# Kernel optimization log

Hardware: AMD Instinct MI355X
Metric: run time of the kernel (lower is better)

The kernel has to match this reference:

```python
import jax, jax.numpy as jnp
import numpy as np
from jax.scipy.special import gammaln

# Problem sizes (static)
N = 50000          # nodes
P = 200000         # paths (source->target pairs in the transitive closure)
L = 6              # edges (nodes) per path -> flat edge list length E = P*L
E = P * L
MAX_DELAY = 128
DT = 1.0
T = int(MAX_DELAY * int(1 / DT))   # expanded time window (== 128)
EPS = 1e-12


def gamma_irf(params):
    """IRF_FN entry: per-node gamma (Nash-cascade) impulse response, [N, T]."""
    a = jax.nn.softplus(params[:, 0]) + 1.0      # shape  > 1
    b = jax.nn.softplus(params[:, 1]) + 0.5      # scale  > 0.5
    t = (jnp.arange(T, dtype=jnp.float32) + 0.5) * jnp.float32(DT)  # [T]
    log_irf = ((a[:, None] - 1.0) * jnp.log(t)[None, :]
               - t[None, :] / b[:, None]
               - gammaln(a)[:, None]
               - a[:, None] * jnp.log(b)[:, None])
    return jnp.exp(log_irf) * jnp.float32(DT)    # [N, T]


def setup_inputs() -> dict:
    key = jax.random.key(0)
    k1, k2 = jax.random.split(key)
    params = jax.random.normal(k1, (N, 2), dtype=jnp.float32)
    edges_flat = jax.random.randint(k2, (E,), 0, N, dtype=jnp.int32)
    path_cumsum = jnp.arange(P + 1, dtype=jnp.int32) * L  # segment offsets into edges_flat
    return {"params": params, "edges_flat": edges_flat, "path_cumsum": path_cumsum}


def reference(params, edges_flat, path_cumsum):
    # --- irf_fn + rfft ---------------------------------------------------
    irfs = gamma_irf(params)                          # [N, T]
    irfs_freq = jnp.fft.rfft(irfs, n=T, axis=-1)      # [N, F] complex64

    # --- log_transitive_closure: product of per-edge spectra along paths -
    log_f = jnp.log(irfs_freq + EPS)                  # complex log, [N, F]
    seg_ids = jnp.searchsorted(path_cumsum[1:], jnp.arange(E, dtype=path_cumsum.dtype),
                               side="right")          # [E] path id per flat edge
    path_log = jax.ops.segment_sum(log_f[edges_flat], seg_ids, num_segments=P)  # [P, F]
    path_freq = jnp.exp(path_log)                     # product along path, [P, F]

    # coords: (source node, target node) of each path; include_index_diag appends (i, i)
    src = edges_flat[path_cumsum[:-1]]
    dst = edges_flat[path_cumsum[1:] - 1]
    diag = jnp.arange(N, dtype=edges_flat.dtype)
    coords = jnp.stack([jnp.concatenate([src, diag]),
                        jnp.concatenate([dst, diag])])              # [2, P+N]
    freq_all = jnp.concatenate([path_freq, irfs_freq], axis=0)      # [P+N, F]

    # --- irfft + postprocessing ------------------------------------------
    irfs_agg = jnp.fft.irfft(freq_all, n=T, axis=-1)  # [P+N, T]
    irfs_agg = jax.nn.relu(irfs_agg)
    # sampler.phi_k: avg-pool by factor int(1/dt) == 1 -> identity when dt=1
    irfs_agg = jnp.flip(irfs_agg, axis=-1)
    irfs_agg = irfs_agg / (jnp.sum(irfs_agg, axis=-1, keepdims=True) + EPS)
    # SparseKernel(coords, values, kernel_size=(N, N, T)) -> return its contents
    return (coords, irfs_agg)
```

## Files before the change

kernel.cpp:

```cpp
#include <hip/hip_runtime.h>
#include <hip/hip_bf16.h>

#define N_NODES 50000
#define P_PATHS 200000
#define N_ROWS  250000
#define L_EDGES 6
#define T_LEN   128
#define F_BINS  65
#define EPSF    1e-12f
#define PIF     3.14159265358979323846f
#define COORD_ELEMS ((size_t)2 * (P_PATHS + N_NODES))
#define FREQ_BYTES  ((size_t)N_NODES * F_BINS * 8)
#define ATILE_OFF   ((size_t)32 * 1024 * 1024)
#define KDIM  128
#define KPADN 128
#define ROWS_BLK 64
#define TILES ((N_ROWS + ROWS_BLK - 1) / ROWS_BLK)
#define GEMM_GRID 1024

typedef _Float16 v2h __attribute__((ext_vector_type(2)));
typedef _Float16 v8h __attribute__((ext_vector_type(8)));
typedef float    v4f __attribute__((ext_vector_type(4)));

__device__ __forceinline__ float softplus_(float x) {
    const float e = __expf(-fabsf(x));
    return fmaxf(x, 0.0f) + __logf(1.0f + e);
}

__device__ __forceinline__ float lgamma_pos_(float x) {
    const float ser = 1.000000000190015f
                    + 76.18009172947146f     / (x + 1.0f)
                    - 86.50532032941677f     / (x + 2.0f)
                    + 24.01409824083091f     / (x + 3.0f)
                    - 1.231739572450155f     / (x + 4.0f)
                    + 0.1208650973866179e-2f / (x + 5.0f)
                    - 0.5395239384953e-5f    / (x + 6.0f);
    const float tmp = x + 5.5f;
    return (x + 0.5f) * __logf(tmp) - tmp + __logf(2.5066282746310005f * ser / x);
}

__global__ void irfa49s_wgen(_Float16* __restrict__ Wt) {
    const int idx = blockIdx.x * 256 + threadIdx.x;
    if (idx >= 128 * KDIM) return;
    const int t  = idx / KDIM;
    const int kk = idx - t * KDIM;
    int j; float cj; bool is_sin;
    if (kk == 1) { j = 64; cj = 1.0f; is_sin = false; }
    else {
        j = kk >> 1;
        cj = (j == 0) ? 1.0f : 2.0f;
        is_sin = (kk & 1);
    }
    const int m = (j * t) & 127;
    const float th = (float)m * (PIF / 64.0f);
    const float tri = is_sin ? -__sinf(th) : __cosf(th);
    Wt[idx] = (_Float16)(cj * tri * (1.0f / 128.0f));
}

__global__ void irfa49s_freq(const float* __restrict__ params, _Float16* __restrict__ freqh) {
    __shared__ float sx[8][T_LEN];
    __shared__ float su[8][64];
    __shared__ float sv[8][64];
    const int tid  = threadIdx.x;
    const int slot = tid >> 5;
    const int tl   = tid & 31;
    const int n    = blockIdx.x * 8 + slot;
    _Float16* fh   = freqh + (size_t)n * KPADN;

    const float a  = softplus_(params[2 * n + 0]) + 1.0f;
    const float b  = softplus_(params[2 * n + 1]) + 0.5f;
    const float lg = lgamma_pos_(a);
    const float lb = __logf(b);
    const float rb = 1.0f / b;
    const float am1 = a - 1.0f;
    const float cst = -lg - a * lb;

    float S = 0.0f;
    #pragma unroll
    for (int j = 0; j < 4; ++j) {
        const float tc = (float)(tl + 32 * j) + 0.5f;
        const float x  = __expf(fmaf(am1, __logf(tc), fmaf(-tc, rb, cst)));
        sx[slot][tl + 32 * j] = x;
        S += x;
    }

    float s0  = S;
    float s64 = (tl & 1) ? -S : S;
    float c32 = ((tl & 3) == 0) ? S : (((tl & 3) == 2) ? -S : 0.0f);
    float s32 = ((tl & 3) == 1) ? S : (((tl & 3) == 3) ? -S : 0.0f);
    #pragma unroll
    for (int m = 16; m; m >>= 1) {
        s0  += __shfl_xor(s0, m);
        s64 += __shfl_xor(s64, m);
        c32 += __shfl_xor(c32, m);
        s32 += __shfl_xor(s32, m);
    }
    __syncthreads();

    {
        const int i1 = tl + 1;
        const float xa = sx[slot][i1], xb = sx[slot][T_LEN - i1];
        su[slot][i1] = xa + xb;
        sv[slot][i1] = xa - xb;
        if (tl < 31) {
            const int i2 = tl + 33;
            const float xc = sx[slot][i2], xd = sx[slot][T_LEN - i2];
            su[slot][i2] = xc + xd;
            sv[slot][i2] = xc - xd;
        }
    }
    __syncthreads();

    if (tl == 0) {
        v2h h;
        h[0] = (_Float16)s0;  h[1] = (_Float16)s64;    *(v2h*)(fh + 0)  = h;
        h[0] = (_Float16)c32; h[1] = (_Float16)(-s32); *(v2h*)(fh + 64) = h;
        return;
    }

    const float x0v  = sx[slot][0];
    const float x64v = sx[slot][64];
    const int   k    = tl;
    const float th   = (float)k * (PIF / 64.0f);
    const float c1 = __cosf(th), s1 = __sinf(th);
    const float c2 = 2.0f * c1 * c1 - 1.0f;
    const float s2 = 2.0f * s1 * c1;
    const float K  = 2.0f * c2;

    float ue1 = 0.0f, ue2 = 0.0f, ve1 = 0.0f, ve2 = 0.0f;
    float uo1 = 0.0f, uo2 = 0.0f, vo1 = 0.0f, vo2 = 0.0f;
    #pragma unroll
    for (int m = 31; m >= 1; --m) {
        const float2 uu = *(const float2*)&su[slot][2 * m];
        const float2 vv = *(const float2*)&sv[slot][2 * m];
        float v0;
        v0 = fmaf(K, ue1, uu.x - ue2); ue2 = ue1; ue1 = v0;
        v0 = fmaf(K, ve1, vv.x - ve2); ve2 = ve1; ve1 = v0;
        v0 = fmaf(K, uo1, uu.y - uo2); uo2 = uo1; uo1 = v0;
        v0 = fmaf(K, vo1, vv.y - vo2); vo2 = vo1; vo1 = v0;
    }
    {
        float v0;
        v0 = fmaf(K, uo1, su[slot][1] - uo2); uo2 = uo1; uo1 = v0;
        v0 = fmaf(K, vo1, sv[slot][1] - vo2); vo2 = vo1; vo1 = v0;
    }

    const float Ec = fmaf(ue1, c2, -ue2);
    const float Es = ve1 * s2;
    const float ReSu = fmaf(-uo2, c2, uo1);
    const float ImSu = uo2 * s2;
    const float Oc   = c1 * ReSu - s1 * ImSu;
    const float ReSv = fmaf(-vo2, c2, vo1);
    const float ImSv = vo2 * s2;
    const float Os   = s1 * ReSv + c1 * ImSv;

    const float base = x0v + ((k & 1) ? -x64v : x64v);
    v2h h;
    h[0] = (_Float16)(base + Ec + Oc);
    h[1] = (_Float16)(-(Es + Os));
    *(v2h*)(fh + 2 * k) = h;
    h[0] = (_Float16)(base + Ec - Oc);
    h[1] = (_Float16)(Es - Os);
    *(v2h*)(fh + 2 * (64 - k)) = h;
}

__global__ __launch_bounds__(256) void irfa49t_prod(const _Float16* __restrict__ freqh,
                                                    const int* __restrict__ edges,
                                                    _Float16* __restrict__ Atile) {
    const int gt  = blockIdx.x * 256 + threadIdx.x;
    const int row = gt >> 5;
    const int tl  = gt & 31;
    _Float16* op = Atile + (size_t)row * KDIM;

    if (row < P_PATHS) {
        const int eb = row * L_EDGES;
        v2h av[L_EDGES], bv[L_EDGES];
        #pragma unroll
        for (int j = 0; j < L_EDGES; ++j) {
            const _Float16* fh = freqh + (size_t)edges[eb + j] * KPADN;
            av[j] = *(const v2h*)(fh + 2 * tl);
            bv[j] = *(const v2h*)(fh + 64 + 2 * tl);
        }
        float p1r = 1.0f, p1i = 0.0f, p2r = 1.0f, p2i = 0.0f, q = 1.0f;
        #pragma unroll
        for (int j = 0; j < L_EDGES; ++j) {
            const float ax  = (float)av[j][0];
            const float ayr = (float)av[j][1];
            const float ay  = (tl == 0) ? 0.0f : ayr;
            float t1 = p1r * ax - p1i * ay;
            p1i      = p1r * ay + p1i * ax;
            p1r = t1;
            q *= ayr;
            const float bx = (float)bv[j][0], by = (float)bv[j][1];
            float t2 = p2r * bx - p2i * by;
            p2i      = p2r * by + p2i * bx;
            p2r = t2;
        }
        v2h h;
        h[0] = (_Float16)p1r;
        h[1] = (tl == 0) ? (_Float16)q : (_Float16)p1i;
        *(v2h*)(op + 2 * tl) = h;
        h[0] = (_Float16)p2r; h[1] = (_Float16)p2i;
        *(v2h*)(op + 64 + 2 * tl) = h;
    } else {
        const _Float16* fh = freqh + (size_t)(row - P_PATHS) * KPADN;
        *(v2h*)(op + 2 * tl)      = *(const v2h*)(fh + 2 * tl);
        *(v2h*)(op + 64 + 2 * tl) = *(const v2h*)(fh + 64 + 2 * tl);
    }
}

__global__ __launch_bounds__(256, 2) void irfa49u_gemm(const _Float16* __restrict__ Atile,
                                                       const _Float16* __restrict__ Wt,
                                                       float* __restrict__ out_agg) {
    const int tid  = threadIdx.x;
    const int wv   = tid >> 6;
    const int lane = tid & 63;
    const int tcol = lane & 15;
    const int kg   = lane >> 4;
    const int rgrp = kg * 4;

    v8h bf[4][8];
    #pragma unroll
    for (int kt = 0; kt < 4; ++kt) {
        #pragma unroll
        for (int nt = 0; nt < 8; ++nt) {
            bf[kt][nt] = *(const v8h*)&Wt[(nt * 16 + tcol) * KDIM + kt * 32 + kg * 8];
        }
    }

    for (int tile = blockIdx.x; tile < TILES; tile += GEMM_GRID) {
        const int rowa = tile * ROWS_BLK + wv * 16 + tcol;
        const _Float16* ap = Atile + (size_t)rowa * KDIM + kg * 8;

        v8h af[4];
        #pragma unroll
        for (int kt = 0; kt < 4; ++kt) af[kt] = *(const v8h*)(ap + kt * 32);

        v4f acc[8];
        #pragma unroll
        for (int nt = 0; nt < 8; ++nt) acc[nt] = (v4f){0.0f, 0.0f, 0.0f, 0.0f};

        #pragma unroll
        for (int kt = 0; kt < 4; ++kt) {
            #pragma unroll
            for (int nt = 0; nt < 8; ++nt) {
                acc[nt] = __builtin_amdgcn_mfma_f32_16x16x32_f16(af[kt], bf[kt][nt], acc[nt], 0, 0, 0);
            }
        }

        #pragma unroll
        for (int reg = 0; reg < 4; ++reg) {
            float vals[8];
            float vsum = 0.0f;
            #pragma unroll
            for (int nt = 0; nt < 8; ++nt) {
                const float v = fmaxf(acc[nt][reg], 0.0f);
                vals[nt] = v;
                vsum += v;
            }
            vsum += __shfl_xor(vsum, 1);
            vsum += __shfl_xor(vsum, 2);
            vsum += __shfl_xor(vsum, 4);
            vsum += __shfl_xor(vsum, 8);
            const int row = tile * ROWS_BLK + wv * 16 + rgrp + reg;
            if (row < N_ROWS) {
                const float inv = 1.0f / (vsum + EPSF);
                float* op = out_agg + (size_t)row * T_LEN;
                #pragma unroll
                for (int nt = 0; nt < 8; ++nt) {
                    const int t = nt * 16 + tcol;
                    op[127 - t] = vals[nt] * inv;
                }
            }
        }
    }
}

__global__ void IRFAggregator_39049842655549_kernel(const int* __restrict__ edges,
                                                    float* __restrict__ out) {
    const int M = P_PATHS + N_NODES;
    const int i = blockIdx.x * blockDim.x + threadIdx.x;
    if (i >= 2 * M) return;
    int v;
    if (i < P_PATHS) {
        v = edges[i * L_EDGES];
    } else if (i < M) {
        v = i - P_PATHS;
    } else {
        const int j = i - M;
        if (j < P_PATHS) v = edges[j * L_EDGES + L_EDGES - 1];
        else             v = j - P_PATHS;
    }
    out[i] = (float)v;
}

extern "C" void kernel_launch(void* const* d_in, const int* in_sizes, int n_in,
                              void* d_out, int out_size, void* d_ws, size_t ws_size,
                              hipStream_t stream) {
    const float* params = (const float*)d_in[0];
    const int*   edges  = (const int*)d_in[1];

    _Float16* freqh = (_Float16*)d_ws;
    _Float16* Wt    = (_Float16*)((char*)d_ws + FREQ_BYTES);
    _Float16* Atile = (_Float16*)((char*)d_ws + ATILE_OFF);
    float* out      = (float*)d_out;
    float* out_agg  = out + COORD_ELEMS;

    IRFAggregator_39049842655549_kernel<<<(int)((COORD_ELEMS + 255) / 256), 256, 0, stream>>>(edges, out);
    irfa49s_wgen<<<(128 * KDIM + 255) / 256, 256, 0, stream>>>(Wt);
    irfa49s_freq<<<N_NODES / 8, 256, 0, stream>>>(params, freqh);
    irfa49t_prod<<<(N_ROWS * 32) / 256, 256, 0, stream>>>(freqh, edges, Atile);
    irfa49u_gemm<<<GEMM_GRID, 256, 0, stream>>>(Atile, Wt, out_agg);
}
```

Measured before the change: 117.0 us.

## Compute per-node forward DFT as fp16 MFMA GEMM instead of Goertzel recurrence

Replaces the per-node shared-memory Goertzel-style forward DFT with a separate IRF generation kernel that writes fp16 time samples to a table, plus an MFMA GEMM against a precomputed cos/sin matrix to produce the spectra. This moves the scalar recurrence onto matrix cores. In exchange it adds a round trip through global memory for the time table, two extra launches, and fp16 rounding of the time samples before the transform.

```diff
diff --git a/kernel.cpp b/kernel.cpp
--- a/kernel.cpp
+++ b/kernel.cpp
@@ -12,11 +12,14 @@
 #define COORD_ELEMS ((size_t)2 * (P_PATHS + N_NODES))
 #define FREQ_BYTES  ((size_t)N_NODES * F_BINS * 8)
 #define ATILE_OFF   ((size_t)32 * 1024 * 1024)
+#define XTAB_OFF    ((size_t)96 * 1024 * 1024)
 #define KDIM  128
 #define KPADN 128
 #define ROWS_BLK 64
 #define TILES ((N_ROWS + ROWS_BLK - 1) / ROWS_BLK)
 #define GEMM_GRID 1024
+#define STILES ((N_NODES + ROWS_BLK - 1) / ROWS_BLK)
+#define SPEC_GRID 391
 
 typedef _Float16 v2h __attribute__((ext_vector_type(2)));
 typedef _Float16 v8h __attribute__((ext_vector_type(8)));
@@ -57,111 +60,89 @@
     Wt[idx] = (_Float16)(cj * tri * (1.0f / 128.0f));
 }
 
-__global__ void irfa49s_freq(const float* __restrict__ params, _Float16* __restrict__ freqh) {
-    __shared__ float sx[8][T_LEN];
-    __shared__ float su[8][64];
-    __shared__ float sv[8][64];
+__global__ void irfa49v_w2gen(_Float16* __restrict__ W2t) {
+    const int idx = blockIdx.x * 256 + threadIdx.x;
+    if (idx >= 128 * 128) return;
+    const int kk = idx >> 7;
+    const int t  = idx & 127;
+    int j; bool is_sin;
+    if (kk == 1) { j = 64; is_sin = false; }
+    else { j = kk >> 1; is_sin = (kk & 1); }
+    const int m = (j * t) & 127;
+    const float th = (float)m * (PIF / 64.0f);
+    W2t[idx] = (_Float16)(is_sin ? -__sinf(th) : __cosf(th));
+}
+
+__global__ __launch_bounds__(256) void irfa49v_xgen(const float* __restrict__ params,
+                                                    _Float16* __restrict__ xtab) {
     const int tid  = threadIdx.x;
-    const int slot = tid >> 5;
-    const int tl   = tid & 31;
-    const int n    = blockIdx.x * 8 + slot;
-    _Float16* fh   = freqh + (size_t)n * KPADN;
-
-    const float a  = softplus_(params[2 * n + 0]) + 1.0f;
-    const float b  = softplus_(params[2 * n + 1]) + 0.5f;
+    const int node = blockIdx.x * 2 + (tid >> 7);
+    const int t    = tid & 127;
+
+    const float a  = softplus_(params[2 * node + 0]) + 1.0f;
+    const float b  = softplus_(params[2 * node + 1]) + 0.5f;
     const float lg = lgamma_pos_(a);
     const float lb = __logf(b);
     const float rb = 1.0f / b;
-    const float am1 = a - 1.0f;
     const float cst = -lg - a * lb;
-
-    float S = 0.0f;
+    const float tc = (float)t + 0.5f;
+    const float x  = __expf(fmaf(a - 1.0f, __logf(tc), fmaf(-tc, rb, cst)));
+    xtab[(size_t)node * T_LEN + t] = (_Float16)x;
+}
+
+__global__ __launch_bounds__(256, 2) void irfa49v_spec(const _Float16* __restrict__ xtab,
+                                                       const _Float16* __restrict__ W2t,
+                                                       _Float16* __restrict__ freqh) {
+    const int tid  = threadIdx.x;
+    const int wv   = tid >> 6;
+    const int lane = tid & 63;
+    const int tcol = lane & 15;
+    const int kg   = lane >> 4;
+    const int rgrp = kg * 4;
+
+    v8h bf[4][8];
     #pragma unroll
-    for (int j = 0; j < 4; ++j) {
-        const float tc = (float)(tl + 32 * j) + 0.5f;
-        const float x  = __expf(fmaf(am1, __logf(tc), fmaf(-tc, rb, cst)));
-        sx[slot][tl + 32 * j] = x;
-        S += x;
-    }
-
-    float s0  = S;
-    float s64 = (tl & 1) ? -S : S;
-    float c32 = ((tl & 3) == 0) ? S : (((tl & 3) == 2) ? -S : 0.0f);
-    float s32 = ((tl & 3) == 1) ? S : (((tl & 3) == 3) ? -S : 0.0f);
-    #pragma unroll
-    for (int m = 16; m; m >>= 1) {
-        s0  += __shfl_xor(s0, m);
-        s64 += __shfl_xor(s64, m);
-        c32 += __shfl_xor(c32, m);
-        s32 += __shfl_xor(s32, m);
-    }
-    __syncthreads();
-
-    {
-        const int i1 = tl + 1;
-        const float xa = sx[slot][i1], xb = sx[slot][T_LEN - i1];
-        su[slot][i1] = xa + xb;
-        sv[slot][i1] = xa - xb;
-        if (tl < 31) {
-            const int i2 = tl + 33;
-            const float xc = sx[slot][i2], xd = sx[slot][T_LEN - i2];
-            su[slot][i2] = xc + xd;
-            sv[slot][i2] = xc - xd;
-        }
-    }
-    __syncthreads();
-
-    if (tl == 0) {
-        v2h h;
-        h[0] = (_Float16)s0;  h[1] = (_Float16)s64;    *(v2h*)(fh + 0)  = h;
-        h[0] = (_Float16)c32; h[1] = (_Float16)(-s32); *(v2h*)(fh + 64) = h;
-        return;
-    }
-
-    const float x0v  = sx[slot][0];
-    const float x64v = sx[slot][64];
-    const int   k    = tl;
-    const float th   = (float)k * (PIF / 64.0f);
-    const float c1 = __cosf(th), s1 = __sinf(th);
-    const float c2 = 2.0f * c1 * c1 - 1.0f;
-    const float s2 = 2.0f * s1 * c1;
-    const float K  = 2.0f * c2;
-
-    float ue1 = 0.0f, ue2 = 0.0f, ve1 = 0.0f, ve2 = 0.0f;
-    float uo1 = 0.0f, uo2 = 0.0f, vo1 = 0.0f, vo2 = 0.0f;
-    #pragma unroll
-    for (int m = 31; m >= 1; --m) {
-        const float2 uu = *(const float2*)&su[slot][2 * m];
-        const float2 vv = *(const float2*)&sv[slot][2 * m];
-        float v0;
-        v0 = fmaf(K, ue1, uu.x - ue2); ue2 = ue1; ue1 = v0;
-        v0 = fmaf(K, ve1, vv.x - ve2); ve2 = ve1; ve1 = v0;
-        v0 = fmaf(K, uo1, uu.y - uo2); uo2 = uo1; uo1 = v0;
-        v0 = fmaf(K, vo1, vv.y - vo2); vo2 = vo1; vo1 = v0;
-    }
-    {
-        float v0;
-        v0 = fmaf(K, uo1, su[slot][1] - uo2); uo2 = uo1; uo1 = v0;
-        v0 = fmaf(K, vo1, sv[slot][1] - vo2); vo2 = vo1; vo1 = v0;
-    }
-
-    const float Ec = fmaf(ue1, c2, -ue2);
-    const float Es = ve1 * s2;
-    const float ReSu = fmaf(-uo2, c2, uo1);
-    const float ImSu = uo2 * s2;
-    const float Oc   = c1 * ReSu - s1 * ImSu;
-    const float ReSv = fmaf(-vo2, c2, vo1);
-    const float ImSv = vo2 * s2;
-    const float Os   = s1 * ReSv + c1 * ImSv;
-
-    const float base = x0v + ((k & 1) ? -x64v : x64v);
-    v2h h;
-    h[0] = (_Float16)(base + Ec + Oc);
-    h[1] = (_Float16)(-(Es + Os));
-    *(v2h*)(fh + 2 * k) = h;
-    h[0] = (_Float16)(base + Ec - Oc);
-    h[1] = (_Float16)(Es - Os);
-    *(v2h*)(fh + 2 * (64 - k)) = h;
+    for (int kt = 0; kt < 4; ++kt) {
+        #pragma unroll
+        for (int nt = 0; nt < 8; ++nt) {
+            bf[kt][nt] = *(const v8h*)&W2t[(nt * 16 + tcol) * 128 + kt * 32 + kg * 8];
+        }
+    }
+
+    for (int tile = blockIdx.x; tile < STILES; tile += SPEC_GRID) {
+        const int rowa = tile * ROWS_BLK + wv * 16 + tcol;
+        v8h af[4];
+        #pragma unroll
+        for (int kt = 0; kt < 4; ++kt) {
+            v8h v = (v8h){(_Float16)0.0f, (_Float16)0.0f, (_Float16)0.0f, (_Float16)0.0f,
+                          (_Float16)0.0f, (_Float16)0.0f, (_Float16)0.0f, (_Float16)0.0f};
+            if (rowa < N_NODES) v = *(const v8h*)&xtab[(size_t)rowa * T_LEN + kt * 32 + kg * 8];
+            af[kt] = v;
+        }
+
+        v4f acc[8];
+        #pragma unroll
+        for (int nt = 0; nt < 8; ++nt) acc[nt] = (v4f){0.0f, 0.0f, 0.0f, 0.0f};
+        #pragma unroll
+        for (int kt = 0; kt < 4; ++kt) {
+            #pragma unroll
+            for (int nt = 0; nt < 8; ++nt) {
+                acc[nt] = __builtin_amdgcn_mfma_f32_16x16x32_f16(af[kt], bf[kt][nt], acc[nt], 0, 0, 0);
+            }
+        }
+
+        #pragma unroll
+        for (int reg = 0; reg < 4; ++reg) {
+            const int row = tile * ROWS_BLK + wv * 16 + rgrp + reg;
+            if (row < N_NODES) {
+                _Float16* op = freqh + (size_t)row * KPADN;
+                #pragma unroll
+                for (int nt = 0; nt < 8; ++nt) {
+                    op[nt * 16 + tcol] = (_Float16)acc[nt][reg];
+                }
+            }
+        }
+    }
 }
 
 __global__ __launch_bounds__(256) void irfa49t_prod(const _Float16* __restrict__ freqh,
@@ -302,13 +283,17 @@
 
     _Float16* freqh = (_Float16*)d_ws;
     _Float16* Wt    = (_Float16*)((char*)d_ws + FREQ_BYTES);
+    _Float16* W2t   = (_Float16*)((char*)d_ws + FREQ_BYTES + 65536);
     _Float16* Atile = (_Float16*)((char*)d_ws + ATILE_OFF);
+    _Float16* xtab  = (_Float16*)((char*)d_ws + XTAB_OFF);
     float* out      = (float*)d_out;
     float* out_agg  = out + COORD_ELEMS;
 
     IRFAggregator_39049842655549_kernel<<<(int)((COORD_ELEMS + 255) / 256), 256, 0, stream>>>(edges, out);
     irfa49s_wgen<<<(128 * KDIM + 255) / 256, 256, 0, stream>>>(Wt);
-    irfa49s_freq<<<N_NODES / 8, 256, 0, stream>>>(params, freqh);
+    irfa49v_w2gen<<<(128 * 128 + 255) / 256, 256, 0, stream>>>(W2t);
+    irfa49v_xgen<<<N_NODES / 2, 256, 0, stream>>>(params, xtab);
+    irfa49v_spec<<<SPEC_GRID, 256, 0, stream>>>(xtab, W2t, freqh);
     irfa49t_prod<<<(N_ROWS * 32) / 256, 256, 0, stream>>>(freqh, edges, Atile);
     irfa49u_gemm<<<GEMM_GRID, 256, 0, stream>>>(Atile, Wt, out_agg);
 }
```

Result: slower. 139.3 us (+19.1%).
